# Kernel tuning notes

Measured on AMD Instinct MI355X. Metric: run time of the kernel, lower is better.

The kernel has to match this reference:

```python
import jax, jax.numpy as jnp
import numpy as np

N, E, G = 100000, 1600000, 64
IN_DIM, EMB, HID, HEADS, OUT = 128, 128, 32, 4, 64
CAT = HID * HEADS  # 128
EPS = 1e-5
SLOPE = 0.2


def gat_conv(x, src, dst, W, a_src, a_dst, bias):
    # x: [N, F_in]; W: [HEADS*HID, F_in]; a_*: [1, HEADS, HID]; bias: [HEADS*HID]
    h = (x @ W.T).reshape(N, HEADS, HID)
    s_src = (h * a_src).sum(-1)  # [N, HEADS]
    s_dst = (h * a_dst).sum(-1)
    e = jax.nn.leaky_relu(s_src[src] + s_dst[dst], SLOPE)  # [Etot, HEADS]
    m = jax.ops.segment_max(e, dst, num_segments=N)
    p = jnp.exp(e - m[dst])
    denom = jax.ops.segment_sum(p, dst, num_segments=N)
    alpha = p / denom[dst]  # softmax over incoming edges per dst node
    out = jax.ops.segment_sum(h[src] * alpha[:, :, None], dst, num_segments=N)
    return out.reshape(N, CAT) + bias


def graph_norm(x, batch, w, b, mean_scale):
    cnt = jax.ops.segment_sum(jnp.ones((N,), x.dtype), batch, num_segments=G)[:, None]
    mean = jax.ops.segment_sum(x, batch, num_segments=G) / cnt  # [G, C]
    sub = x - mean_scale * mean[batch]
    var = jax.ops.segment_sum(sub * sub, batch, num_segments=G) / cnt
    inv = 1.0 / jnp.sqrt(var + EPS)
    return w * sub * inv[batch] + b


def setup_inputs() -> dict:
    key = jax.random.key(0)
    ks = jax.random.split(key, 20)
    g = lambda k, shape, s: jax.random.normal(k, shape, dtype=jnp.float32) * s
    inp = {
        'x': g(ks[0], (N, IN_DIM), 1.0),
        'edge_index': jax.random.randint(ks[1], (2, E), 0, N, dtype=jnp.int64 if jax.config.read('jax_enable_x64') else jnp.int32),
        'batch': jnp.sort(jax.random.randint(ks[2], (N,), 0, G)),
        'enc_w': g(ks[3], (EMB, IN_DIM), 0.08),
        'enc_b': jnp.zeros((EMB,), jnp.float32),
        'w1': g(ks[4], (HEADS * HID, EMB), 0.08),
        'att_src1': g(ks[5], (1, HEADS, HID), 0.15),
        'att_dst1': g(ks[6], (1, HEADS, HID), 0.15),
        'b1': jnp.zeros((CAT,), jnp.float32),
        'n1_w': jnp.ones((CAT,), jnp.float32),
        'n1_b': jnp.zeros((CAT,), jnp.float32),
        'n1_ms': jnp.ones((CAT,), jnp.float32),
        'w2': g(ks[7], (HEADS * HID, CAT), 0.08),
        'att_src2': g(ks[8], (1, HEADS, HID), 0.15),
        'att_dst2': g(ks[9], (1, HEADS, HID), 0.15),
        'b2': jnp.zeros((CAT,), jnp.float32),
        'n2_w': jnp.ones((CAT,), jnp.float32),
        'n2_b': jnp.zeros((CAT,), jnp.float32),
        'n2_ms': jnp.ones((CAT,), jnp.float32),
        'fc_w': g(ks[10], (OUT, CAT), 0.08),
        'fc_b': jnp.zeros((OUT,), jnp.float32),
    }
    return inp


def reference(x, edge_index, batch, enc_w, enc_b, w1, att_src1, att_dst1, b1,
              n1_w, n1_b, n1_ms, w2, att_src2, att_dst2, b2, n2_w, n2_b, n2_ms,
              fc_w, fc_b):
    # PyG GATConv adds self-loops by default
    loops = jnp.arange(N, dtype=edge_index.dtype)
    src = jnp.concatenate([edge_index[0], loops])
    dst = jnp.concatenate([edge_index[1], loops])

    h = x @ enc_w.T + enc_b
    h = jax.nn.elu(gat_conv(h, src, dst, w1, att_src1, att_dst1, b1))
    h = graph_norm(h, batch, n1_w, n1_b, n1_ms)  # dropout = identity (eval)
    h = jax.nn.elu(gat_conv(h, src, dst, w2, att_src2, att_dst2, b2))
    h = graph_norm(h, batch, n2_w, n2_b, n2_ms)
    pooled = jax.ops.segment_max(h, batch, num_segments=G)  # global_max_pool
    return pooled @ fc_w.T + fc_b  # out_dim != 1 -> no sigmoid
```

## Files before the change

### kernel.cpp

```cpp
#include <hip/hip_runtime.h>
#include <hip/hip_bf16.h>

#define SLOPE 0.2f
#define EPS_GN 1e-5f
#define APITCH 136
#define NBUCK 391

typedef __attribute__((ext_vector_type(8))) short bfrag;
typedef __attribute__((ext_vector_type(4))) float ffrag;

__device__ __forceinline__ float lrelu(float v) { return v > 0.f ? v : SLOPE * v; }
__device__ __forceinline__ short f2bs(float v) {
    __hip_bfloat16 h = __float2bfloat16(v);
    return *reinterpret_cast<short*>(&h);
}
__device__ __forceinline__ float blo(unsigned int u) { return __uint_as_float(u << 16); }
__device__ __forceinline__ float bhi(unsigned int u) { return __uint_as_float(u & 0xffff0000u); }

__global__ void __launch_bounds__(256) setup_kernel(
    const int* __restrict__ ei, int* __restrict__ bhist, int E, int N, int EB,
    const float* __restrict__ enc_w, const float* __restrict__ enc_b,
    const float* __restrict__ w1, const float* __restrict__ w2,
    unsigned short* __restrict__ WT1b, unsigned short* __restrict__ WT2b,
    float* __restrict__ bc1, float* __restrict__ bc2) {
    __shared__ int shmem[NBUCK];
    int tid = threadIdx.x;
    if ((int)blockIdx.x < EB) {
        for (int i = tid; i < NBUCK; i += 256) shmem[i] = 0;
        __syncthreads();
        int base = blockIdx.x * 4096;
#pragma unroll
        for (int s = 0; s < 16; ++s) {
            int e = base + s * 256 + tid;
            if (e < E + N) {
                int dst = (e < E) ? ei[E + e] : (e - E);
                atomicAdd(&shmem[dst >> 8], 1);
            }
        }
        __syncthreads();
        for (int i = tid; i < NBUCK; i += 256)
            if (shmem[i]) atomicAdd(&bhist[i], shmem[i]);
    } else {
        int c = blockIdx.x - EB;
        float* w1row = (float*)shmem;
        if (tid < 128) w1row[tid] = w1[c * 128 + tid];
        __syncthreads();
        if (tid < 128) {
            int k = tid;
            float acc = 0.f;
            for (int j = 0; j < 128; ++j)
                acc = fmaf(w1row[j], enc_w[j * 128 + k], acc);
            WT1b[c * 128 + k] = (unsigned short)f2bs(acc);
            WT2b[c * 128 + k] = (unsigned short)f2bs(w2[c * 128 + k]);
            if (k == 0) {
                float b = 0.f;
                for (int j = 0; j < 128; ++j) b += w1row[j] * enc_b[j];
                bc1[c] = b;
                bc2[c] = 0.f;
            }
        }
    }
}


__global__ void bucket_scan(const int* __restrict__ bhist,
                            int* __restrict__ bbase, int* __restrict__ bcur) {
    __shared__ int sh[512];
    int t = threadIdx.x;
    int v = (t < NBUCK) ? bhist[t] : 0;
    sh[t] = v;
    __syncthreads();
    for (int off = 1; off < 512; off <<= 1) {
        int add = (t >= off) ? sh[t - off] : 0;
        __syncthreads();
        sh[t] += add;
        __syncthreads();
    }
    if (t < NBUCK) {
        bbase[t] = sh[t] - v;
        bcur[t] = sh[t] - v;
    }
}

__global__ void __launch_bounds__(256) bucket_scatter(const int* __restrict__ ei,
                                                      int* __restrict__ bcur,
                                                      unsigned int* __restrict__ staging,
                                                      int E, int N) {
    __shared__ int h[NBUCK];
    __shared__ int lb[NBUCK];
    for (int i = threadIdx.x; i < NBUCK; i += 256) h[i] = 0;
    __syncthreads();
    int base = blockIdx.x * 4096;
    int srcv[16], dstv[16];
#pragma unroll
    for (int s = 0; s < 16; ++s) {
        int e = base + s * 256 + threadIdx.x;
        srcv[s] = -1;
        if (e < E + N) {
            srcv[s] = (e < E) ? ei[e] : (e - E);
            dstv[s] = (e < E) ? ei[E + e] : (e - E);
            atomicAdd(&h[dstv[s] >> 8], 1);
        }
    }
    __syncthreads();
    for (int i = threadIdx.x; i < NBUCK; i += 256) {
        int c = h[i];
        lb[i] = c ? atomicAdd(&bcur[i], c) : 0;
        h[i] = 0;
    }
    __syncthreads();
#pragma unroll
    for (int s = 0; s < 16; ++s) {
        if (srcv[s] >= 0) {
            int b = dstv[s] >> 8;
            int slot = atomicAdd(&h[b], 1);
            staging[lb[b] + slot] = ((unsigned int)srcv[s] << 8) | (unsigned int)(dstv[s] & 255);
        }
    }
}

__global__ void __launch_bounds__(256) bucket_finalize(
    const unsigned int* __restrict__ staging,
    const int* __restrict__ bbase, const int* __restrict__ bcur,
    int* __restrict__ rowp, int* __restrict__ esrc, int N, int Etot) {
    int b = blockIdx.x, t = threadIdx.x;
    __shared__ int h[256], sc[256];
    h[t] = 0;
    __syncthreads();
    int s0 = bbase[b], s1 = bcur[b];
    for (int j = s0 + t; j < s1; j += 256)
        atomicAdd(&h[staging[j] & 255], 1);
    __syncthreads();
    int d = h[t];
    sc[t] = d;
    __syncthreads();
    for (int off = 1; off < 256; off <<= 1) {
        int add = (t >= off) ? sc[t - off] : 0;
        __syncthreads();
        sc[t] += add;
        __syncthreads();
    }
    int excl = s0 + sc[t] - d;
    int node = b * 256 + t;
    if (node < N) rowp[node] = excl;
    if (b == 0 && t == 0) rowp[N] = Etot;
    __syncthreads();
    h[t] = excl;
    __syncthreads();
    for (int j = s0 + t; j < s1; j += 256) {
        unsigned int p = staging[j];
        int pos = atomicAdd(&h[p & 255], 1);
        esrc[pos] = (int)(p >> 8);
    }
}

__global__ void __launch_bounds__(256) gemm_mfma(
    const void* __restrict__ Ain, const unsigned short* __restrict__ WTb,
    const float* __restrict__ bias, const float* __restrict__ att_src,
    const float* __restrict__ att_dst, const int* __restrict__ batch,
    const float* __restrict__ Ac, const float* __restrict__ Bc,
    unsigned int* __restrict__ H, float* __restrict__ ssrc, float* __restrict__ sdst, int N) {
    __shared__ short Csh[64 * APITCH];
    __shared__ float asrc_s[128], adst_s[128], bias_s[128];
    int tid = threadIdx.x;
    int base = blockIdx.x * 64;
    if (tid < 128) {
        asrc_s[tid] = att_src[tid];
        adst_s[tid] = att_dst[tid];
        bias_s[tid] = bias[tid];
    }

    int w = tid >> 6, lane = tid & 63, col = lane & 15, quad = lane >> 4;
    int rowBase = w * 16;
    int node = base + rowBase + col;
    bool valid = node < N;

    bfrag afr[4];
    if (Ac == nullptr) {
        const float* A = (const float*)Ain;
#pragma unroll
        for (int s = 0; s < 4; ++s) {
            short o[8] = {0, 0, 0, 0, 0, 0, 0, 0};
            if (valid) {
                int k8 = s * 32 + quad * 8;
                float4 v0 = *(const float4*)&A[(size_t)node * 128 + k8];
                float4 v1 = *(const float4*)&A[(size_t)node * 128 + k8 + 4];
                o[0] = f2bs(v0.x); o[1] = f2bs(v0.y); o[2] = f2bs(v0.z); o[3] = f2bs(v0.w);
                o[4] = f2bs(v1.x); o[5] = f2bs(v1.y); o[6] = f2bs(v1.z); o[7] = f2bs(v1.w);
            }
            afr[s] = *(bfrag*)o;
        }
    } else {
        const uint4* A4 = (const uint4*)Ain;
        int g = valid ? batch[node] : 0;
#pragma unroll
        for (int s = 0; s < 4; ++s) {
            short o[8] = {0, 0, 0, 0, 0, 0, 0, 0};
            if (valid) {
                int k8 = s * 32 + quad * 8;
                uint4 hb = A4[(size_t)node * 16 + s * 4 + quad];
                float4 a0 = *(const float4*)&Ac[g * 128 + k8];
                float4 a1 = *(const float4*)&Ac[g * 128 + k8 + 4];
                float4 b0 = *(const float4*)&Bc[g * 128 + k8];
                float4 b1 = *(const float4*)&Bc[g * 128 + k8 + 4];
                o[0] = f2bs(fmaf(blo(hb.x), a0.x, b0.x));
                o[1] = f2bs(fmaf(bhi(hb.x), a0.y, b0.y));
                o[2] = f2bs(fmaf(blo(hb.y), a0.z, b0.z));
                o[3] = f2bs(fmaf(bhi(hb.y), a0.w, b0.w));
                o[4] = f2bs(fmaf(blo(hb.z), a1.x, b1.x));
                o[5] = f2bs(fmaf(bhi(hb.z), a1.y, b1.y));
                o[6] = f2bs(fmaf(blo(hb.w), a1.z, b1.z));
                o[7] = f2bs(fmaf(bhi(hb.w), a1.w, b1.w));
            }
            afr[s] = *(bfrag*)o;
        }
    }

    ffrag acc[8];
#pragma unroll
    for (int t = 0; t < 8; ++t) acc[t] = (ffrag){0.f, 0.f, 0.f, 0.f};

#pragma unroll
    for (int t = 0; t < 8; ++t) {
#pragma unroll
        for (int s = 0; s < 4; ++s) {
            bfrag bfr = *(const bfrag*)&WTb[(t * 16 + col) * 128 + s * 32 + quad * 8];
            acc[t] = __builtin_amdgcn_mfma_f32_16x16x32_bf16(afr[s], bfr, acc[t], 0, 0, 0);
        }
    }

    __syncthreads();
#pragma unroll
    for (int t = 0; t < 8; ++t) {
        int ch = t * 16 + col;
        float bv = bias_s[ch];
#pragma unroll
        for (int r = 0; r < 4; ++r)
            Csh[(rowBase + quad * 4 + r) * APITCH + ch] = f2bs(acc[t][r] + bv);
    }
    __syncthreads();

    float2 av = make_float2(asrc_s[lane * 2], asrc_s[lane * 2 + 1]);
    float2 dv = make_float2(adst_s[lane * 2], adst_s[lane * 2 + 1]);
    for (int r = 0; r < 16; ++r) {
        int n2 = base + rowBase + r;
        unsigned int hb = *(const unsigned int*)&Csh[(rowBase + r) * APITCH + lane * 2];
        float hx = blo(hb);
        float hy = bhi(hb);
        float vs = hx * av.x + hy * av.y;
        float vd = hx * dv.x + hy * dv.y;
#pragma unroll
        for (int off = 8; off; off >>= 1) {
            vs += __shfl_xor(vs, off, 16);
            vd += __shfl_xor(vd, off, 16);
        }
        if (n2 < N) {
            H[n2 * 64 + lane] = hb;
            if ((lane & 15) == 0) {
                int h = lane >> 4;
                ssrc[n2 * 4 + h] = vs;
                sdst[n2 * 4 + h] = vd;
            }
        }
    }
}

__global__ void __launch_bounds__(256) agg_kernel(
    const int* __restrict__ row, const int* __restrict__ esrc,
    const float* __restrict__ ssrc, const float* __restrict__ sdst,
    const uint4* __restrict__ H4, const float* __restrict__ bias,
    uint4* __restrict__ out, int N) {
    int n = (blockIdx.x * 256 + threadIdx.x) >> 6;
    int lane = threadIdx.x & 63;
    if (n >= N) return;
    int slot = lane >> 4, li = lane & 15, head = li >> 2;
    int beg = row[n], end = row[n + 1];
    float sdh = sdst[n * 4 + head];

    float num[8] = {0.f, 0.f, 0.f, 0.f, 0.f, 0.f, 0.f, 0.f};
    float den = 0.f;
    for (int e = beg + slot; e < end; e += 4) {
        int s = esrc[e];
        float al = __expf(lrelu(ssrc[s * 4 + head] + sdh));
        uint4 hb = H4[s * 16 + li];
        den += al;
        num[0] = fmaf(al, blo(hb.x), num[0]);
        num[1] = fmaf(al, bhi(hb.x), num[1]);
        num[2] = fmaf(al, blo(hb.y), num[2]);
        num[3] = fmaf(al, bhi(hb.y), num[3]);
        num[4] = fmaf(al, blo(hb.z), num[4]);
        num[5] = fmaf(al, bhi(hb.z), num[5]);
        num[6] = fmaf(al, blo(hb.w), num[6]);
        num[7] = fmaf(al, bhi(hb.w), num[7]);
    }
    den += __shfl_xor(den, 16);
    den += __shfl_xor(den, 32);
#pragma unroll
    for (int j = 0; j < 8; ++j) {
        num[j] += __shfl_xor(num[j], 16);
        num[j] += __shfl_xor(num[j], 32);
    }
    if (slot == 0) {
        float rh = 1.f / den;
        int c0 = li * 8;
        unsigned int o[4];
#pragma unroll
        for (int p = 0; p < 4; ++p) {
            float v0 = fmaf(num[2 * p], rh, bias[c0 + 2 * p]);
            float v1 = fmaf(num[2 * p + 1], rh, bias[c0 + 2 * p + 1]);
            v0 = v0 > 0.f ? v0 : __expf(v0) - 1.f;
            v1 = v1 > 0.f ? v1 : __expf(v1) - 1.f;
            o[p] = ((unsigned int)(unsigned short)f2bs(v0)) |
                   (((unsigned int)(unsigned short)f2bs(v1)) << 16);
        }
        out[n * 16 + li] = make_uint4(o[0], o[1], o[2], o[3]);
    }
}

template <int POOL>
__global__ void __launch_bounds__(256) stats_kernel(
    const uint4* __restrict__ X4, const int* __restrict__ batch,
    float* __restrict__ part, int N) {
    __shared__ float red[16][16][9];
    int t = threadIdx.x, u4 = t & 15, rg = t >> 4;
    int base = blockIdx.x * 64;
    int g0 = batch[base];

    float s[2][8] = {}, q[2][8] = {};
    float mx[2][8], mn[2][8];
#pragma unroll
    for (int st = 0; st < 2; ++st)
#pragma unroll
        for (int p = 0; p < 8; ++p) { mx[st][p] = -3e38f; mn[st][p] = 3e38f; }

#pragma unroll
    for (int rr = 0; rr < 4; ++rr) {
        int node = base + rg + rr * 16;
        if (node < N) {
            uint4 hb = X4[node * 16 + u4];
            int st = (batch[node] != g0) ? 1 : 0;
            float vv[8] = {blo(hb.x), bhi(hb.x), blo(hb.y), bhi(hb.y),
                           blo(hb.z), bhi(hb.z), blo(hb.w), bhi(hb.w)};
#pragma unroll
            for (int p = 0; p < 8; ++p) {
                s[st][p] += vv[p];
                q[st][p] += vv[p] * vv[p];
                if (POOL) {
                    mx[st][p] = fmaxf(mx[st][p], vv[p]);
                    mn[st][p] = fminf(mn[st][p], vv[p]);
                }
            }
        }
    }

    int uu = t >> 3, ch = t & 7;
    float rs[2] = {0.f, 0.f}, rq[2] = {0.f, 0.f};
    float rmx[2] = {-3e38f, -3e38f}, rmn[2] = {3e38f, 3e38f};
    for (int st = 0; st < 2; ++st) {
#pragma unroll
        for (int p = 0; p < 8; ++p) red[rg][u4][p] = s[st][p];
        __syncthreads();
        if (t < 128) { float a = 0.f; for (int r2 = 0; r2 < 16; ++r2) a += red[r2][uu][ch]; rs[st] = a; }
        __syncthreads();
#pragma unroll
        for (int p = 0; p < 8; ++p) red[rg][u4][p] = q[st][p];
        __syncthreads();
        if (t < 128) { float a = 0.f; for (int r2 = 0; r2 < 16; ++r2) a += red[r2][uu][ch]; rq[st] = a; }
        __syncthreads();
        if (POOL) {
#pragma unroll
            for (int p = 0; p < 8; ++p) red[rg][u4][p] = mx[st][p];
            __syncthreads();
            if (t < 128) { float a = -3e38f; for (int r2 = 0; r2 < 16; ++r2) a = fmaxf(a, red[r2][uu][ch]); rmx[st] = a; }
            __syncthreads();
#pragma unroll
            for (int p = 0; p < 8; ++p) red[rg][u4][p] = mn[st][p];
            __syncthreads();
            if (t < 128) { float a = 3e38f; for (int r2 = 0; r2 < 16; ++r2) a = fminf(a, red[r2][uu][ch]); rmn[st] = a; }
            __syncthreads();
        }
    }
    if (t < 128) {
        float* pb = part + (size_t)blockIdx.x * 8 * 128;
        pb[0 * 128 + t] = rs[0];
        pb[1 * 128 + t] = rq[0];
        pb[2 * 128 + t] = rs[1];
        pb[3 * 128 + t] = rq[1];
        if (POOL) {
            pb[4 * 128 + t] = rmx[0];
            pb[5 * 128 + t] = rmn[0];
            pb[6 * 128 + t] = rmx[1];
            pb[7 * 128 + t] = rmn[1];
        }
    }
}

__global__ void reduce_coef(const float* __restrict__ part,
                            const int* __restrict__ batch, int N,
                            const float* __restrict__ w, const float* __restrict__ b,
                            const float* __restrict__ ms,
                            float* __restrict__ Ac, float* __restrict__ Bc) {
    __shared__ int sh2[2];
    int g = blockIdx.x, c = threadIdx.x;
    if (c < 2) {
        int key = g + c;
        int lo = 0, hi = N;
        while (lo < hi) { int m = (lo + hi) >> 1; if (batch[m] < key) lo = m + 1; else hi = m; }
        sh2[c] = lo;
    }
    __syncthreads();
    int sidx = sh2[0], eidx = sh2[1];
    float cnt = (float)(eidx - sidx);
    if (cnt < 0.5f) { Ac[g * 128 + c] = 0.f; Bc[g * 128 + c] = 0.f; return; }
    int b0 = sidx >> 6, b1 = (eidx - 1) >> 6;
    float s = 0.f, q = 0.f;
    for (int bb = b0; bb <= b1; ++bb) {
        int g0b = batch[bb << 6];
        int qoff;
        bool take;
        if (g0b == g) { qoff = 0; take = true; }
        else {
            int g1b = batch[min((bb << 6) + 63, N - 1)];
            take = (g1b == g);
            qoff = 2;
        }
        if (take) {
            const float* pb = part + (size_t)bb * 8 * 128;
            s += pb[qoff * 128 + c];
            q += pb[(qoff + 1) * 128 + c];
        }
    }
    float mean = s / cnt;
    float msv = ms[c];
    float var = q / cnt - msv * (2.f - msv) * mean * mean;
    var = fmaxf(var, 0.f);
    float inv = rsqrtf(var + EPS_GN);
    float a = w[c] * inv;
    Ac[g * 128 + c] = a;
    Bc[g * 128 + c] = b[c] - msv * mean * a;
}

__global__ void __launch_bounds__(128) reduce_fc(
    const float* __restrict__ part, const int* __restrict__ batch, int N,
    const float* __restrict__ w, const float* __restrict__ b,
    const float* __restrict__ ms,
    const float* __restrict__ fcw, const float* __restrict__ fcb,
    float* __restrict__ out) {
    __shared__ int sh2[2];
    __shared__ float p[128];
    int g = blockIdx.x, c = threadIdx.x;
    if (c < 2) {
        int key = g + c;
        int lo = 0, hi = N;
        while (lo < hi) { int m = (lo + hi) >> 1; if (batch[m] < key) lo = m + 1; else hi = m; }
        sh2[c] = lo;
    }
    __syncthreads();
    int sidx = sh2[0], eidx = sh2[1];
    float cnt = (float)(eidx - sidx);
    if (cnt < 0.5f) {
        p[c] = 0.f;
    } else {
        int b0 = sidx >> 6, b1 = (eidx - 1) >> 6;
        float s = 0.f, q = 0.f, M = -3e38f, m = 3e38f;
        for (int bb = b0; bb <= b1; ++bb) {
            int g0b = batch[bb << 6];
            int qoff;
            bool take;
            if (g0b == g) { qoff = 0; take = true; }
            else {
                int g1b = batch[min((bb << 6) + 63, N - 1)];
                take = (g1b == g);
                qoff = 2;
            }
            if (take) {
                const float* pb = part + (size_t)bb * 8 * 128;
                s += pb[qoff * 128 + c];
                q += pb[(qoff + 1) * 128 + c];
                M = fmaxf(M, pb[(4 + qoff) * 128 + c]);
                m = fminf(m, pb[(5 + qoff) * 128 + c]);
            }
        }
        float mean = s / cnt;
        float msv = ms[c];
        float var = q / cnt - msv * (2.f - msv) * mean * mean;
        var = fmaxf(var, 0.f);
        float inv = rsqrtf(var + EPS_GN);
        float a = w[c] * inv;
        float bb2 = b[c] - msv * mean * a;
        p[c] = (a >= 0.f) ? fmaf(a, M, bb2) : fmaf(a, m, bb2);
    }
    __syncthreads();
    if (c < 64) {
        float acc = fcb[c];
        for (int k = 0; k < 128; ++k)
            acc = fmaf(p[k], fcw[c * 128 + k], acc);
        out[g * 64 + c] = acc;
    }
}

extern "C" void kernel_launch(void* const* d_in, const int* in_sizes, int n_in,
                              void* d_out, int out_size, void* d_ws, size_t ws_size,
                              hipStream_t stream) {
    const float* x     = (const float*)d_in[0];
    const int* ei      = (const int*)d_in[1];
    const int* batch   = (const int*)d_in[2];
    const float* enc_w = (const float*)d_in[3];
    const float* enc_b = (const float*)d_in[4];
    const float* w1    = (const float*)d_in[5];
    const float* as1   = (const float*)d_in[6];
    const float* ad1   = (const float*)d_in[7];
    const float* b1    = (const float*)d_in[8];
    const float* n1w   = (const float*)d_in[9];
    const float* n1b   = (const float*)d_in[10];
    const float* n1ms  = (const float*)d_in[11];
    const float* w2    = (const float*)d_in[12];
    const float* as2   = (const float*)d_in[13];
    const float* ad2   = (const float*)d_in[14];
    const float* b2    = (const float*)d_in[15];
    const float* n2w   = (const float*)d_in[16];
    const float* n2b   = (const float*)d_in[17];
    const float* n2ms  = (const float*)d_in[18];
    const float* fcw   = (const float*)d_in[19];
    const float* fcb   = (const float*)d_in[20];
    float* out = (float*)d_out;

    int N = in_sizes[2];
    int E = in_sizes[1] / 2;
    int Etot = E + N;
    int SB = (N + 63) / 64;
    int EB = (Etot + 4095) / 4096;

    char* ws = (char*)d_ws;
    size_t off = 0;
    auto take = [&](size_t bytes) {
        char* p = ws + off;
        off = (off + bytes + 255) & ~(size_t)255;
        return p;
    };
    unsigned short* WT1b = (unsigned short*)take(128 * 128 * 2);
    unsigned short* WT2b = (unsigned short*)take(128 * 128 * 2);
    float* bc1 = (float*)take(512);
    float* bc2 = (float*)take(512);
    float* ssrc = (float*)take((size_t)N * 16);
    float* sdst = (float*)take((size_t)N * 16);
    int* rowp   = (int*)take((size_t)(N + 1) * 4);
    int* esrc   = (int*)take((size_t)Etot * 4);
    unsigned int* staging = (unsigned int*)take((size_t)Etot * 4);
    int* bbase  = (int*)take(512 * 4);
    int* bcur   = (int*)take(512 * 4);
    int* bhist  = (int*)take(512 * 4);
    unsigned int* H = (unsigned int*)take((size_t)N * 256);
    unsigned int* AG = (unsigned int*)take((size_t)N * 256);
    float* Ac   = (float*)take(64 * 128 * 4);
    float* Bc   = (float*)take(64 * 128 * 4);
    float* part = (float*)take((size_t)SB * 8 * 128 * 4);
    if (off > ws_size) return;

    hipMemsetAsync(bhist, 0, 512 * 4, stream);
    setup_kernel<<<EB + 128, 256, 0, stream>>>(ei, bhist, E, N, EB,
                                               enc_w, enc_b, w1, w2,
                                               WT1b, WT2b, bc1, bc2);
    bucket_scan<<<1, 512, 0, stream>>>(bhist, bbase, bcur);
    bucket_scatter<<<EB, 256, 0, stream>>>(ei, bcur, staging, E, N);
    bucket_finalize<<<NBUCK, 256, 0, stream>>>(staging, bbase, bcur, rowp, esrc, N, Etot);

    gemm_mfma<<<(N + 63) / 64, 256, 0, stream>>>(x, WT1b, bc1, as1, ad1, batch,
                                                 nullptr, nullptr, H, ssrc, sdst, N);
    agg_kernel<<<(N + 3) / 4, 256, 0, stream>>>(rowp, esrc, ssrc, sdst,
                                                (const uint4*)H, b1, (uint4*)AG, N);
    stats_kernel<0><<<SB, 256, 0, stream>>>((const uint4*)AG, batch, part, N);
    reduce_coef<<<64, 128, 0, stream>>>(part, batch, N, n1w, n1b, n1ms, Ac, Bc);

    gemm_mfma<<<(N + 63) / 64, 256, 0, stream>>>(AG, WT2b, bc2, as2, ad2, batch,
                                                 Ac, Bc, H, ssrc, sdst, N);
    agg_kernel<<<(N + 3) / 4, 256, 0, stream>>>(rowp, esrc, ssrc, sdst,
                                                (const uint4*)H, b2, (uint4*)AG, N);
    stats_kernel<1><<<SB, 256, 0, stream>>>((const uint4*)AG, batch, part, N);
    reduce_fc<<<64, 128, 0, stream>>>(part, batch, N, n2w, n2b, n2ms, fcw, fcb, out);
}
```

Baseline: 473.8 us.

## Split node features into channel-sliced planes and aggregate per slice

After: 840.4 us. 1.77x slower.

```diff
diff --git a/kernel.cpp b/kernel.cpp
--- a/kernel.cpp
+++ b/kernel.cpp
@@ -62,7 +62,6 @@
     }
 }
 
-
 __global__ void bucket_scan(const int* __restrict__ bhist,
                             int* __restrict__ bbase, int* __restrict__ bcur) {
     __shared__ int sh[512];
@@ -159,11 +158,12 @@
     const float* __restrict__ bias, const float* __restrict__ att_src,
     const float* __restrict__ att_dst, const int* __restrict__ batch,
     const float* __restrict__ Ac, const float* __restrict__ Bc,
-    unsigned int* __restrict__ H, float* __restrict__ ssrc, float* __restrict__ sdst, int N) {
+    unsigned int* __restrict__ Hp, float* __restrict__ ssrc, float* __restrict__ sdst, int N) {
     __shared__ short Csh[64 * APITCH];
     __shared__ float asrc_s[128], adst_s[128], bias_s[128];
     int tid = threadIdx.x;
     int base = blockIdx.x * 64;
+    size_t PS = (size_t)N * 8;
     if (tid < 128) {
         asrc_s[tid] = att_src[tid];
         adst_s[tid] = att_dst[tid];
@@ -191,14 +191,14 @@
             afr[s] = *(bfrag*)o;
         }
     } else {
-        const uint4* A4 = (const uint4*)Ain;
+        const unsigned int* A1 = (const unsigned int*)Ain;
         int g = valid ? batch[node] : 0;
 #pragma unroll
         for (int s = 0; s < 4; ++s) {
             short o[8] = {0, 0, 0, 0, 0, 0, 0, 0};
             if (valid) {
                 int k8 = s * 32 + quad * 8;
-                uint4 hb = A4[(size_t)node * 16 + s * 4 + quad];
+                uint4 hb = *(const uint4*)&A1[(size_t)(k8 >> 4) * PS + (size_t)node * 8 + ((k8 & 15) >> 1)];
                 float4 a0 = *(const float4*)&Ac[g * 128 + k8];
                 float4 a1 = *(const float4*)&Ac[g * 128 + k8 + 4];
                 float4 b0 = *(const float4*)&Bc[g * 128 + k8];
@@ -242,6 +242,7 @@
 
     float2 av = make_float2(asrc_s[lane * 2], asrc_s[lane * 2 + 1]);
     float2 dv = make_float2(adst_s[lane * 2], adst_s[lane * 2 + 1]);
+    int plane = lane >> 3, pl8 = lane & 7;
     for (int r = 0; r < 16; ++r) {
         int n2 = base + rowBase + r;
         unsigned int hb = *(const unsigned int*)&Csh[(rowBase + r) * APITCH + lane * 2];
@@ -255,11 +256,11 @@
             vd += __shfl_xor(vd, off, 16);
         }
         if (n2 < N) {
-            H[n2 * 64 + lane] = hb;
+            Hp[(size_t)plane * PS + (size_t)n2 * 8 + pl8] = hb;
             if ((lane & 15) == 0) {
                 int h = lane >> 4;
-                ssrc[n2 * 4 + h] = vs;
-                sdst[n2 * 4 + h] = vd;
+                ssrc[(size_t)h * N + n2] = vs;
+                sdst[(size_t)h * N + n2] = vd;
             }
         }
     }
@@ -268,63 +269,53 @@
 __global__ void __launch_bounds__(256) agg_kernel(
     const int* __restrict__ row, const int* __restrict__ esrc,
     const float* __restrict__ ssrc, const float* __restrict__ sdst,
-    const uint4* __restrict__ H4, const float* __restrict__ bias,
-    uint4* __restrict__ out, int N) {
-    int n = (blockIdx.x * 256 + threadIdx.x) >> 6;
+    const unsigned int* __restrict__ Hp, const float* __restrict__ bias,
+    unsigned int* __restrict__ outp, int N) {
+    int slice = blockIdx.x & 7;
+    int n = (blockIdx.x >> 3) * 4 + (threadIdx.x >> 6);
+    if (n >= N) return;
     int lane = threadIdx.x & 63;
-    if (n >= N) return;
-    int slot = lane >> 4, li = lane & 15, head = li >> 2;
+    int slot = lane >> 3, li = lane & 7;
+    int head = slice >> 1;
     int beg = row[n], end = row[n + 1];
-    float sdh = sdst[n * 4 + head];
-
-    float num[8] = {0.f, 0.f, 0.f, 0.f, 0.f, 0.f, 0.f, 0.f};
-    float den = 0.f;
-    for (int e = beg + slot; e < end; e += 4) {
+    float sdh = sdst[(size_t)head * N + n];
+    const unsigned int* Hpl = Hp + (size_t)slice * N * 8;
+    const float* ssr = ssrc + (size_t)head * N;
+
+    float num0 = 0.f, num1 = 0.f, den = 0.f;
+    for (int e = beg + slot; e < end; e += 8) {
         int s = esrc[e];
-        float al = __expf(lrelu(ssrc[s * 4 + head] + sdh));
-        uint4 hb = H4[s * 16 + li];
+        float al = __expf(lrelu(ssr[s] + sdh));
+        unsigned int hb = Hpl[(size_t)s * 8 + li];
         den += al;
-        num[0] = fmaf(al, blo(hb.x), num[0]);
-        num[1] = fmaf(al, bhi(hb.x), num[1]);
-        num[2] = fmaf(al, blo(hb.y), num[2]);
-        num[3] = fmaf(al, bhi(hb.y), num[3]);
-        num[4] = fmaf(al, blo(hb.z), num[4]);
-        num[5] = fmaf(al, bhi(hb.z), num[5]);
-        num[6] = fmaf(al, blo(hb.w), num[6]);
-        num[7] = fmaf(al, bhi(hb.w), num[7]);
-    }
-    den += __shfl_xor(den, 16);
-    den += __shfl_xor(den, 32);
-#pragma unroll
-    for (int j = 0; j < 8; ++j) {
-        num[j] += __shfl_xor(num[j], 16);
-        num[j] += __shfl_xor(num[j], 32);
-    }
+        num0 = fmaf(al, blo(hb), num0);
+        num1 = fmaf(al, bhi(hb), num1);
+    }
+    den += __shfl_xor(den, 8);  den += __shfl_xor(den, 16);  den += __shfl_xor(den, 32);
+    num0 += __shfl_xor(num0, 8); num0 += __shfl_xor(num0, 16); num0 += __shfl_xor(num0, 32);
+    num1 += __shfl_xor(num1, 8); num1 += __shfl_xor(num1, 16); num1 += __shfl_xor(num1, 32);
     if (slot == 0) {
         float rh = 1.f / den;
-        int c0 = li * 8;
-        unsigned int o[4];
-#pragma unroll
-        for (int p = 0; p < 4; ++p) {
-            float v0 = fmaf(num[2 * p], rh, bias[c0 + 2 * p]);
-            float v1 = fmaf(num[2 * p + 1], rh, bias[c0 + 2 * p + 1]);
-            v0 = v0 > 0.f ? v0 : __expf(v0) - 1.f;
-            v1 = v1 > 0.f ? v1 : __expf(v1) - 1.f;
-            o[p] = ((unsigned int)(unsigned short)f2bs(v0)) |
-                   (((unsigned int)(unsigned short)f2bs(v1)) << 16);
-        }
-        out[n * 16 + li] = make_uint4(o[0], o[1], o[2], o[3]);
+        int c0 = slice * 16 + li * 2;
+        float v0 = fmaf(num0, rh, bias[c0]);
+        float v1 = fmaf(num1, rh, bias[c0 + 1]);
+        v0 = v0 > 0.f ? v0 : __expf(v0) - 1.f;
+        v1 = v1 > 0.f ? v1 : __expf(v1) - 1.f;
+        outp[(size_t)slice * N * 8 + (size_t)n * 8 + li] =
+            ((unsigned int)(unsigned short)f2bs(v0)) |
+            (((unsigned int)(unsigned short)f2bs(v1)) << 16);
     }
 }
 
 template <int POOL>
 __global__ void __launch_bounds__(256) stats_kernel(
-    const uint4* __restrict__ X4, const int* __restrict__ batch,
+    const unsigned int* __restrict__ Xp, const int* __restrict__ batch,
     float* __restrict__ part, int N) {
     __shared__ float red[16][16][9];
     int t = threadIdx.x, u4 = t & 15, rg = t >> 4;
     int base = blockIdx.x * 64;
     int g0 = batch[base];
+    size_t PS = (size_t)N * 8;
 
     float s[2][8] = {}, q[2][8] = {};
     float mx[2][8], mn[2][8];
@@ -337,7 +328,7 @@
     for (int rr = 0; rr < 4; ++rr) {
         int node = base + rg + rr * 16;
         if (node < N) {
-            uint4 hb = X4[node * 16 + u4];
+            uint4 hb = *(const uint4*)&Xp[(size_t)(u4 >> 1) * PS + (size_t)node * 8 + (u4 & 1) * 4];
             int st = (batch[node] != g0) ? 1 : 0;
             float vv[8] = {blo(hb.x), bhi(hb.x), blo(hb.y), bhi(hb.y),
                            blo(hb.z), bhi(hb.z), blo(hb.w), bhi(hb.w)};
@@ -565,17 +556,17 @@
     bucket_scatter<<<EB, 256, 0, stream>>>(ei, bcur, staging, E, N);
     bucket_finalize<<<NBUCK, 256, 0, stream>>>(staging, bbase, bcur, rowp, esrc, N, Etot);
 
+    int AGG_B = ((N + 3) / 4) * 8;
+
     gemm_mfma<<<(N + 63) / 64, 256, 0, stream>>>(x, WT1b, bc1, as1, ad1, batch,
                                                  nullptr, nullptr, H, ssrc, sdst, N);
-    agg_kernel<<<(N + 3) / 4, 256, 0, stream>>>(rowp, esrc, ssrc, sdst,
-                                                (const uint4*)H, b1, (uint4*)AG, N);
-    stats_kernel<0><<<SB, 256, 0, stream>>>((const uint4*)AG, batch, part, N);
+    agg_kernel<<<AGG_B, 256, 0, stream>>>(rowp, esrc, ssrc, sdst, H, b1, AG, N);
+    stats_kernel<0><<<SB, 256, 0, stream>>>(AG, batch, part, N);
     reduce_coef<<<64, 128, 0, stream>>>(part, batch, N, n1w, n1b, n1ms, Ac, Bc);
 
     gemm_mfma<<<(N + 63) / 64, 256, 0, stream>>>(AG, WT2b, bc2, as2, ad2, batch,
                                                  Ac, Bc, H, ssrc, sdst, N);
-    agg_kernel<<<(N + 3) / 4, 256, 0, stream>>>(rowp, esrc, ssrc, sdst,
-                                                (const uint4*)H, b2, (uint4*)AG, N);
-    stats_kernel<1><<<SB, 256, 0, stream>>>((const uint4*)AG, batch, part, N);
+    agg_kernel<<<AGG_B, 256, 0, stream>>>(rowp, esrc, ssrc, sdst, H, b2, AG, N);
+    stats_kernel<1><<<SB, 256, 0, stream>>>(AG, batch, part, N);
     reduce_fc<<<64, 128, 0, stream>>>(part, batch, N, n2w, n2b, n2ms, fcw, fcb, out);
 }
```
